# Kernel optimization log

Hardware: AMD Instinct MI355X
Metric: run time of the kernel (lower is better)

Reference implementation:

```python
import jax, jax.numpy as jnp
import numpy as np

B, T, DMODEL, H, DK, DV, FF = 4, 1024, 1024, 16, 64, 64, 4096


def _weight_mask(dmodel, dk):
    # tril ones -> 0 on/below diag, -inf above (matches torch masked_fill)
    m = jnp.tril(jnp.ones((dmodel, dk), dtype=jnp.float32))
    return jnp.where(m == 0, -jnp.inf, 0.0).astype(jnp.float32)


def _mha(Q, K, V, Wq, Wk, Wv, Wo, maskout):
    dk = Wq.shape[-1]
    if maskout:
        mask = _weight_mask(Wq.shape[1], dk)[None]  # (1, dmodel, dk)
        # softmax over the dmodel axis of the masked weight tensors (axis -2)
        Wq = jax.nn.softmax(Wq + mask, axis=-2)
        Wk = jax.nn.softmax(Wk + mask, axis=-2)
    WqQ = jnp.einsum('btd,hdk->bhtk', Q, Wq)
    WkK = jnp.einsum('btd,hdk->bhtk', K, Wk)
    WvV = jnp.einsum('btd,hdv->bhtv', V, Wv)
    scores = jnp.einsum('bhtk,bhsk->bhts', WqQ, WkK) / jnp.sqrt(jnp.float32(dk))
    # NOTE: source softmaxes over axis -2 (the QUERY axis), not the key axis
    attn = jax.nn.softmax(scores, axis=-2)
    out = jnp.einsum('bhts,bhsv->bhtv', attn, WvV)
    b, h, t, dv = out.shape
    out = out.transpose(0, 2, 1, 3).reshape(b, t, h * dv)  # (B, T, dmodel)
    return out @ Wo


def _norm(x):
    mean = jnp.mean(x, axis=-1, keepdims=True)
    std = jnp.std(x, axis=-1, keepdims=True, ddof=1)  # torch.std is unbiased
    return (x - mean) / std


def setup_inputs() -> dict:
    key = jax.random.key(0)
    ks = jax.random.split(key, 14)
    s = 0.02
    return {
        'x': jax.random.normal(ks[0], (B, T, DMODEL), jnp.float32),
        'y': jax.random.normal(ks[1], (B, T, DMODEL), jnp.float32),
        'Wq1': jax.random.normal(ks[2], (H, DMODEL, DK), jnp.float32) * s,
        'Wk1': jax.random.normal(ks[3], (H, DMODEL, DK), jnp.float32) * s,
        'Wv1': jax.random.normal(ks[4], (H, DMODEL, DV), jnp.float32) * s,
        'Wo1': jax.random.normal(ks[5], (DMODEL, DMODEL), jnp.float32) * s,
        'Wq2': jax.random.normal(ks[6], (H, DMODEL, DK), jnp.float32) * s,
        'Wk2': jax.random.normal(ks[7], (H, DMODEL, DK), jnp.float32) * s,
        'Wv2': jax.random.normal(ks[8], (H, DMODEL, DV), jnp.float32) * s,
        'Wo2': jax.random.normal(ks[9], (DMODEL, DMODEL), jnp.float32) * s,
        'w_in': jax.random.normal(ks[10], (FF, DMODEL), jnp.float32) * s,
        'b_in': jax.random.normal(ks[11], (FF,), jnp.float32) * s,
        'w_out': jax.random.normal(ks[12], (DMODEL, FF), jnp.float32) * s,
        'b_out': jax.random.normal(ks[13], (DMODEL,), jnp.float32) * s,
    }


def reference(x, y, Wq1, Wk1, Wv1, Wo1, Wq2, Wk2, Wv2, Wo2, w_in, b_in, w_out, b_out):
    # masked self-attention on decoded seq y
    out1 = _norm(_mha(y, y, y, Wq1, Wk1, Wv1, Wo1, True) + y)
    # cross-attention against encoded seq x
    out2 = _norm(_mha(out1, x, x, Wq2, Wk2, Wv2, Wo2, False) + out1)
    ff = jax.nn.relu(out2 @ w_in.T + b_in) @ w_out.T + b_out
    out3 = _norm(ff + out2)
    return (x, out3)
```

## Files before the change

kernel.cpp:

```cpp
#include <hip/hip_runtime.h>
#include <hip/hip_bf16.h>

#define BB 4
#define TT 1024
#define DD 1024
#define HH 16
#define DKK 64
#define FFF 4096

typedef unsigned short u16;
typedef unsigned int u32;
typedef __attribute__((ext_vector_type(8))) short s16x8;
typedef __attribute__((ext_vector_type(4))) float f32x4;

static __device__ __forceinline__ float bf2f(u16 s) {
  union { u32 u; float f; } v; v.u = ((u32)s) << 16; return v.f;
}
static __device__ __forceinline__ u16 f2bf(float f) {
  union { float f; u32 u; } v; v.f = f;
  u32 r = v.u + 0x7FFFu + ((v.u >> 16) & 1u);
  return (u16)(r >> 16);
}

#define GLDS(gp, lp) __builtin_amdgcn_global_load_lds( \
    (const __attribute__((address_space(1))) u32*)(gp), \
    (__attribute__((address_space(3))) u32*)(lp), 16, 0, 0)

static __device__ __forceinline__ void swz_block(int& bx, int& by) {
  int gx = gridDim.x, gy = gridDim.y;
  int nwg = gx * gy;
  int orig = by * gx + bx;
  int q = nwg >> 3, r = nwg & 7;
  int xcd = orig & 7, sl = orig >> 3;
  int wgid = (xcd < r ? xcd * (q + 1) : r * (q + 1) + (xcd - r) * q) + sl;
  int g = gx << 3;
  int grp = wgid / g, rem = wgid % g;
  bx = rem >> 3;
  by = (grp << 3) + (rem & 7);
}

static __device__ __forceinline__ void swz_attn(int& tileIdx, int& bh) {
  int orig = blockIdx.y * 8 + blockIdx.x;
  int wgid = ((orig & 7) << 6) | (orig >> 3);
  tileIdx = wgid & 7;
  bh = wgid >> 3;
}

__global__ __launch_bounds__(256) void k_f2bf(const float* __restrict__ s, u16* __restrict__ d, int n) {
  int i = (blockIdx.x * 256 + threadIdx.x) * 4;
  if (i < n) {
    float4 v = *(const float4*)(s + i);
    u16 o[4] = { f2bf(v.x), f2bf(v.y), f2bf(v.z), f2bf(v.w) };
    *(ushort4*)(d + i) = *(ushort4*)o;
  }
}

__global__ __launch_bounds__(256) void k_combine_bf(const u16* __restrict__ a, const u16* __restrict__ b,
                                                    u16* __restrict__ d, int n) {
  int i = (blockIdx.x * 256 + threadIdx.x) * 4;
  if (i < n) {
    ushort4 va = *(const ushort4*)(a + i);
    ushort4 vb = *(const ushort4*)(b + i);
    u16 o[4] = { f2bf(bf2f(va.x) + bf2f(vb.x)), f2bf(bf2f(va.y) + bf2f(vb.y)),
                 f2bf(bf2f(va.z) + bf2f(vb.z)), f2bf(bf2f(va.w) + bf2f(vb.w)) };
    *(ushort4*)(d + i) = *(ushort4*)o;
  }
}

__global__ __launch_bounds__(256) void k_xprep(const float* __restrict__ x, float* __restrict__ dout,
                                               u16* __restrict__ xb, int n) {
  int i = (blockIdx.x * 256 + threadIdx.x) * 4;
  if (i < n) {
    float4 v = *(const float4*)(x + i);
    *(float4*)(dout + i) = v;
    u16 o[4] = { f2bf(v.x), f2bf(v.y), f2bf(v.z), f2bf(v.w) };
    *(ushort4*)(xb + i) = *(ushort4*)o;
  }
}

__global__ __launch_bounds__(256) void k_softmax_w_bf(const float* __restrict__ W, u16* __restrict__ Bt) {
  int col = blockIdx.x;
  int h = col >> 6, k = col & 63;
  int tid = threadIdx.x;
  const float* w = W + ((size_t)h * DD) * DKK + k;
  __shared__ float red[256];
  float m = -1e30f;
  for (int d = k + tid; d < DD; d += 256) m = fmaxf(m, w[(size_t)d * DKK]);
  red[tid] = m; __syncthreads();
  for (int s = 128; s > 0; s >>= 1) { if (tid < s) red[tid] = fmaxf(red[tid], red[tid + s]); __syncthreads(); }
  m = red[0]; __syncthreads();
  float sum = 0.f;
  for (int d = k + tid; d < DD; d += 256) sum += __expf(w[(size_t)d * DKK] - m);
  red[tid] = sum; __syncthreads();
  for (int s = 128; s > 0; s >>= 1) { if (tid < s) red[tid] += red[tid + s]; __syncthreads(); }
  float inv = 1.f / red[0];
  for (int d = tid; d < DD; d += 256) {
    float v = (d >= k) ? __expf(w[(size_t)d * DKK] - m) * inv : 0.f;
    Bt[(size_t)col * DD + d] = f2bf(v);
  }
}

__global__ __launch_bounds__(256) void k_reorder_w_bf(const float* __restrict__ W, u16* __restrict__ Bt) {
  int d0 = blockIdx.x << 6, h = blockIdx.y;
  __shared__ float t[64][65];
  int tid = threadIdx.x;
  const float* src = W + (size_t)h * DD * DKK + (size_t)d0 * DKK;
  #pragma unroll
  for (int i = 0; i < 16; ++i) {
    int e = i * 256 + tid; int r = e >> 6, c = e & 63;
    t[r][c] = src[(size_t)r * DKK + c];
  }
  __syncthreads();
  #pragma unroll
  for (int i = 0; i < 16; ++i) {
    int e = i * 256 + tid; int c = e >> 6, r = e & 63;
    Bt[((size_t)(h * 64 + c)) * DD + d0 + r] = f2bf(t[r][c]);
  }
}

__global__ __launch_bounds__(256) void k_transpose_bf(const float* __restrict__ W, u16* __restrict__ Bt) {
  int k0 = blockIdx.x << 6, n0 = blockIdx.y << 6;
  __shared__ float t[64][65];
  int tid = threadIdx.x;
  #pragma unroll
  for (int i = 0; i < 16; ++i) {
    int e = i * 256 + tid; int r = e >> 6, c = e & 63;
    t[r][c] = W[(size_t)(k0 + r) * DD + n0 + c];
  }
  __syncthreads();
  #pragma unroll
  for (int i = 0; i < 16; ++i) {
    int e = i * 256 + tid; int c = e >> 6, r = e & 63;
    Bt[(size_t)(n0 + c) * DD + k0 + r] = f2bf(t[r][c]);
  }
}

__global__ __launch_bounds__(512) void k_mfma_nt(
    const u16* __restrict__ A, const u16* __restrict__ B,
    u16* __restrict__ P0, u16* __restrict__ P1, u16* __restrict__ P2, u16* __restrict__ P3,
    u16* __restrict__ Cb, u16* __restrict__ Cb2, u16* __restrict__ Ct,
    const float* __restrict__ bias, int relu, int mode, int M, int N, int K) {
  __shared__ u16 SLDS[24576];
  int bx = blockIdx.x, by = blockIdx.y;
  swz_block(bx, by);
  int tid = threadIdx.x, wave = tid >> 6, lane = tid & 63;
  int row0 = by << 7, col0 = bx << 7;
  int wm = (wave >> 2) << 6;
  int wn = (wave & 3) << 5;

  int Ksl = K / gridDim.z;
  int kbase = blockIdx.z * Ksl;
  int nt = Ksl >> 5;

  f32x4 acc[4][2];
  #pragma unroll
  for (int m = 0; m < 4; ++m)
    #pragma unroll
    for (int n = 0; n < 2; ++n) acc[m][n] = f32x4{0.f, 0.f, 0.f, 0.f};

  int srow = tid >> 2, scol = (tid & 3) << 3;
  const u16* Ag = A + (size_t)(row0 + srow) * K + scol;
  const u16* Bg = B + (size_t)(col0 + srow) * K + scol;
  int wbase = wave << 9;

  int fr = lane & 15, kg = (lane >> 4) << 3;
  int ardo = (wm + fr) * 32 + kg;
  int brdo = 12288 + (wn + fr) * 32 + kg;

  auto STAGE = [&](int buf, int k0) {
    GLDS(Ag + k0, SLDS + buf * 4096 + wbase);
    GLDS(Bg + k0, SLDS + 12288 + buf * 4096 + wbase);
  };

  STAGE(0, kbase);
  if (nt > 1) STAGE(1, kbase + 32);
  int bufT = 0;
  for (int t = 0; t < nt; ++t) {
    if (t + 1 < nt) asm volatile("s_waitcnt vmcnt(2)" ::: "memory");
    else            asm volatile("s_waitcnt vmcnt(0)" ::: "memory");
    __builtin_amdgcn_s_barrier();
    asm volatile("" ::: "memory");
    if (t + 2 < nt) {
      int b2 = bufT + 2; if (b2 >= 3) b2 -= 3;
      STAGE(b2, kbase + (t + 2) * 32);
    }
    const u16* Ard = SLDS + bufT * 4096 + ardo;
    const u16* Brd = SLDS + bufT * 4096 + brdo;
    s16x8 aF[4], bF[2];
    #pragma unroll
    for (int m = 0; m < 4; ++m) aF[m] = *(const s16x8*)(Ard + m * 16 * 32);
    #pragma unroll
    for (int n = 0; n < 2; ++n) bF[n] = *(const s16x8*)(Brd + n * 16 * 32);
    #pragma unroll
    for (int m = 0; m < 4; ++m)
      #pragma unroll
      for (int n = 0; n < 2; ++n)
        acc[m][n] = __builtin_amdgcn_mfma_f32_16x16x32_bf16(aF[m], bF[n], acc[m][n], 0, 0, 0);
    ++bufT; if (bufT == 3) bufT = 0;
  }
  __syncthreads();

  int fq = (lane >> 4) << 2;

  u16* dstRow = nullptr; u16* dstCol = nullptr;
  int rowPitch = 1024, colBase = col0 & 1023;
  if (mode == 0) {
    rowPitch = N; colBase = col0;
    if (gridDim.z > 1) {
      int z = blockIdx.z;
      dstRow = (z == 0) ? P0 : ((z == 1) ? P1 : ((z == 2) ? P2 : P3));
    } else dstRow = Cb;
  }
  else if (mode == 1) { int q = col0 >> 10; if (q == 0) dstRow = Cb; else if (q == 1) dstRow = Cb2; else dstCol = Ct; }
  else { int q = col0 >> 10; if (q == 0) dstRow = Cb; else dstCol = Ct; }

  u16* Ep = SLDS + wave * 2048;
  #pragma unroll
  for (int m = 0; m < 4; ++m) {
    #pragma unroll
    for (int n = 0; n < 2; ++n) {
      int col = col0 + wn + n * 16 + fr;
      float bs = bias ? bias[col] : 0.f;
      #pragma unroll
      for (int r = 0; r < 4; ++r) {
        float v = acc[m][n][r] + bs;
        if (relu) v = fmaxf(v, 0.f);
        Ep[(fq + r) * 40 + n * 16 + fr] = f2bf(v);
      }
    }
    if (dstRow) {
      int rw = lane >> 2, seg = lane & 3;
      const u16* src = Ep + rw * 40 + seg * 8;
      u16* gd = dstRow + (size_t)(row0 + wm + m * 16 + rw) * rowPitch + colBase + wn + seg * 8;
      *(uint4*)gd = *(const uint4*)src;
    } else {
      int c = lane >> 1, half = lane & 1;
      u16 tmp[8];
      #pragma unroll
      for (int j = 0; j < 8; ++j) tmp[j] = Ep[(half * 8 + j) * 40 + c];
      u16* gd = dstCol + (size_t)(colBase + wn + c) * 4096 + row0 + wm + m * 16 + half * 8;
      *(uint4*)gd = *(const uint4*)tmp;
    }
  }
}

static __device__ __forceinline__ void stage_tile512(const u16* __restrict__ g, int gp, u16* L, int tid) {
  int row = tid >> 3, col8 = (tid & 7) << 3;
  *(uint4*)(L + row * 72 + col8) = *(const uint4*)(g + (size_t)row * gp + col8);
}

__global__ __launch_bounds__(512) void k_attn_stats_mfma(const u16* __restrict__ Qb, const u16* __restrict__ Kb,
                                                         float* __restrict__ csum) {
  __shared__ u16 Ks[2 * 4608];
  __shared__ u16 Qs[4608];
  int tid = threadIdx.x, wave = tid >> 6, lane = tid & 63;
  int tileIdx, bh;
  swz_attn(tileIdx, bh);
  int b = bh >> 4, h = bh & 15;
  int s0 = tileIdx << 7;
  int tile = wave >> 2, sw = wave & 3;
  stage_tile512(Kb + ((size_t)(b * TT + s0)) * DD + h * 64, DD, Ks, tid);
  stage_tile512(Kb + ((size_t)(b * TT + s0 + 64)) * DD + h * 64, DD, Ks + 4608, tid);
  int row = tid >> 3, col8 = (tid & 7) << 3;
  const u16* Qg = Qb + ((size_t)(b * TT) + row) * DD + h * 64 + col8;
  uint4 qreg = *(const uint4*)Qg;
  __syncthreads();
  int fr = lane & 15, g = lane >> 4;
  const u16* Bbase = Ks + tile * 4608 + (sw * 16 + fr) * 72 + g * 8;
  const u16* Abase = Qs + fr * 72 + g * 8;
  s16x8 bF0 = *(const s16x8*)(Bbase);
  s16x8 bF1 = *(const s16x8*)(Bbase + 32);
  float sum = 0.f;
  for (int t0 = 0; t0 < TT; t0 += 64) {
    __syncthreads();
    *(uint4*)(Qs + row * 72 + col8) = qreg;
    __syncthreads();
    if (t0 + 64 < TT) qreg = *(const uint4*)(Qg + (size_t)(t0 + 64) * DD);
    #pragma unroll
    for (int mt = 0; mt < 4; ++mt) {
      f32x4 acc = f32x4{0.f, 0.f, 0.f, 0.f};
      s16x8 a0 = *(const s16x8*)(Abase + mt * 16 * 72);
      s16x8 a1 = *(const s16x8*)(Abase + mt * 16 * 72 + 32);
      acc = __builtin_amdgcn_mfma_f32_16x16x32_bf16(a0, bF0, acc, 0, 0, 0);
      acc = __builtin_amdgcn_mfma_f32_16x16x32_bf16(a1, bF1, acc, 0, 0, 0);
      sum += __expf(acc[0] * 0.125f) + __expf(acc[1] * 0.125f)
           + __expf(acc[2] * 0.125f) + __expf(acc[3] * 0.125f);
    }
  }
  sum += __shfl_xor(sum, 16, 64);
  sum += __shfl_xor(sum, 32, 64);
  if (lane < 16) csum[(size_t)bh * TT + s0 + tile * 64 + sw * 16 + lane] = sum;
}

__global__ __launch_bounds__(512) void k_attn_apply_mfma(const u16* __restrict__ Qb, const u16* __restrict__ Kb,
                                                         const u16* __restrict__ Vt,
                                                         const float* __restrict__ csum,
                                                         u16* __restrict__ Op) {
  __shared__ u16 Qs[2 * 4608];
  __shared__ u16 KV2[2 * 4608];
  __shared__ u16 Pl[8 * 1024];
  __shared__ float rcsL[64];
  u16* Ks = KV2;
  u16* VTs = KV2 + 4608;
  int tid = threadIdx.x, wave = tid >> 6, lane = tid & 63;
  int tileIdx, bh;
  swz_attn(tileIdx, bh);
  int b = bh >> 4, h = bh & 15;
  int t0 = tileIdx << 7;
  int tile = wave >> 2, tw = wave & 3;
  stage_tile512(Qb + ((size_t)(b * TT + t0)) * DD + h * 64, DD, Qs, tid);
  stage_tile512(Qb + ((size_t)(b * TT + t0 + 64)) * DD + h * 64, DD, Qs + 4608, tid);
  int row = tid >> 3, col8 = (tid & 7) << 3;
  const u16* Kg = Kb + ((size_t)(b * TT) + row) * DD + h * 64 + col8;
  const u16* Vg = Vt + ((size_t)(h * 64) + row) * 4096 + (size_t)b * TT + col8;
  const size_t cbase = (size_t)bh * TT;
  uint4 kreg = *(const uint4*)Kg;
  uint4 vreg = *(const uint4*)Vg;
  float rc0 = (tid < 64) ? csum[cbase + tid] : 0.f;
  __syncthreads();
  int fr = lane & 15, g = lane >> 4;
  const u16* QbF = Qs + tile * 4608 + (tw * 16 + fr) * 72 + g * 8;
  const u16* KaF = Ks + fr * 72 + g * 8;
  char* Pw = (char*)(Pl + wave * 1024);
  uint swz = ((uint)(lane & 7)) << 4;
  s16x8 qF0 = *(const s16x8*)(QbF);
  s16x8 qF1 = *(const s16x8*)(QbF + 32);
  f32x4 acc_o[4];
  #pragma unroll
  for (int nt = 0; nt < 4; ++nt) acc_o[nt] = f32x4{0.f, 0.f, 0.f, 0.f};

  for (int s0 = 0; s0 < TT; s0 += 64) {
    __syncthreads();
    *(uint4*)(Ks + row * 72 + col8) = kreg;
    *(uint4*)(VTs + row * 72 + col8) = vreg;
    if (tid < 64) rcsL[tid] = 1.f / rc0;
    __syncthreads();
    if (s0 + 64 < TT) {
      kreg = *(const uint4*)(Kg + (size_t)(s0 + 64) * DD);
      vreg = *(const uint4*)(Vg + s0 + 64);
      if (tid < 64) rc0 = csum[cbase + s0 + 64 + tid];
    }
    #pragma unroll
    for (int mt = 0; mt < 4; ++mt) {
      f32x4 acc = f32x4{0.f, 0.f, 0.f, 0.f};
      s16x8 a0 = *(const s16x8*)(KaF + mt * 16 * 72);
      s16x8 a1 = *(const s16x8*)(KaF + mt * 16 * 72 + 32);
      acc = __builtin_amdgcn_mfma_f32_16x16x32_bf16(a0, qF0, acc, 0, 0, 0);
      acc = __builtin_amdgcn_mfma_f32_16x16x32_bf16(a1, qF1, acc, 0, 0, 0);
      f32x4 rc4 = *(const f32x4*)&rcsL[mt * 16 + g * 4];
      u16 pb[4];
      #pragma unroll
      for (int r = 0; r < 4; ++r)
        pb[r] = f2bf(__expf(acc[r] * 0.125f) * rc4[r]);
      uint woff = (uint)fr * 128 + (uint)(mt * 16 + g * 4) * 2;
      uint2 wv; wv.x = (u32)pb[0] | ((u32)pb[1] << 16); wv.y = (u32)pb[2] | ((u32)pb[3] << 16);
      *(uint2*)(Pw + (woff ^ swz)) = wv;
    }
    uint rbase = (uint)fr * 128;
    s16x8 pF0 = *(const s16x8*)(Pw + ((rbase + g * 16) ^ swz));
    s16x8 pF1 = *(const s16x8*)(Pw + ((rbase + 64 + g * 16) ^ swz));
    #pragma unroll
    for (int nt = 0; nt < 4; ++nt) {
      s16x8 v0 = *(const s16x8*)(VTs + (nt * 16 + fr) * 72 + g * 8);
      s16x8 v1 = *(const s16x8*)(VTs + (nt * 16 + fr) * 72 + 32 + g * 8);
      acc_o[nt] = __builtin_amdgcn_mfma_f32_16x16x32_bf16(pF0, v0, acc_o[nt], 0, 0, 0);
      acc_o[nt] = __builtin_amdgcn_mfma_f32_16x16x32_bf16(pF1, v1, acc_o[nt], 0, 0, 0);
    }
  }
  __syncthreads();
  u16* Ep = KV2 + wave * 1088;
  #pragma unroll
  for (int nt = 0; nt < 4; ++nt)
    #pragma unroll
    for (int r = 0; r < 4; ++r)
      Ep[(g * 4 + r) * 68 + nt * 16 + fr] = f2bf(acc_o[nt][r]);
  {
    int rw = lane >> 2, seg = lane & 3;
    const u16* src = Ep + rw * 68 + seg * 16;
    u16* gd = Op + ((size_t)(b * TT + t0 + tile * 64 + tw * 16 + rw)) * DD + h * 64 + seg * 16;
    #pragma unroll
    for (int i = 0; i < 4; ++i) *(uint2*)(gd + i * 4) = *(const uint2*)(src + i * 4);
  }
}

__global__ __launch_bounds__(256) void k_add_norm(const u16* __restrict__ A, const u16* __restrict__ A2,
                                                  const u16* __restrict__ A3, const u16* __restrict__ A4,
                                                  const float* __restrict__ bias,
                                                  const float* __restrict__ Bv,
                                                  float* __restrict__ O, u16* __restrict__ Ob) {
  int row = blockIdx.x, tid = threadIdx.x;
  size_t base = (size_t)row * DD;
  int c0 = tid * 4;
  __shared__ float red[256];
  float v[4];
  {
    ushort4 a = *(const ushort4*)(A + base + c0);
    float4 bv = *(const float4*)(Bv + base + c0);
    v[0] = bf2f(a.x) + bv.x; v[1] = bf2f(a.y) + bv.y;
    v[2] = bf2f(a.z) + bv.z; v[3] = bf2f(a.w) + bv.w;
  }
  if (A2) {
    ushort4 a = *(const ushort4*)(A2 + base + c0);
    v[0] += bf2f(a.x); v[1] += bf2f(a.y); v[2] += bf2f(a.z); v[3] += bf2f(a.w);
  }
  if (A3) {
    ushort4 a = *(const ushort4*)(A3 + base + c0);
    v[0] += bf2f(a.x); v[1] += bf2f(a.y); v[2] += bf2f(a.z); v[3] += bf2f(a.w);
  }
  if (A4) {
    ushort4 a = *(const ushort4*)(A4 + base + c0);
    v[0] += bf2f(a.x); v[1] += bf2f(a.y); v[2] += bf2f(a.z); v[3] += bf2f(a.w);
  }
  if (bias) {
    float4 bs = *(const float4*)(bias + c0);
    v[0] += bs.x; v[1] += bs.y; v[2] += bs.z; v[3] += bs.w;
  }
  float s = v[0] + v[1] + v[2] + v[3];
  red[tid] = s; __syncthreads();
  for (int t = 128; t > 0; t >>= 1) { if (tid < t) red[tid] += red[tid + t]; __syncthreads(); }
  float mean = red[0] * (1.f / 1024.f);
  __syncthreads();
  float vs = 0.f;
  #pragma unroll
  for (int i = 0; i < 4; ++i) { float d = v[i] - mean; vs += d * d; }
  red[tid] = vs; __syncthreads();
  for (int t = 128; t > 0; t >>= 1) { if (tid < t) red[tid] += red[tid + t]; __syncthreads(); }
  float inv = rsqrtf(red[0] * (1.f / 1023.f));
  float o[4];
  #pragma unroll
  for (int i = 0; i < 4; ++i) o[i] = (v[i] - mean) * inv;
  *(float4*)(O + base + c0) = *(float4*)o;
  if (Ob) {
    u16 ob[4] = { f2bf(o[0]), f2bf(o[1]), f2bf(o[2]), f2bf(o[3]) };
    *(ushort4*)(Ob + base + c0) = *(ushort4*)ob;
  }
}

extern "C" void kernel_launch(void* const* d_in, const int* in_sizes, int n_in,
                              void* d_out, int out_size, void* d_ws, size_t ws_size,
                              hipStream_t stream) {
  (void)in_sizes; (void)n_in; (void)out_size; (void)ws_size;
  const float* x    = (const float*)d_in[0];
  const float* y    = (const float*)d_in[1];
  const float* Wq1  = (const float*)d_in[2];
  const float* Wk1  = (const float*)d_in[3];
  const float* Wv1  = (const float*)d_in[4];
  const float* Wo1  = (const float*)d_in[5];
  const float* Wq2  = (const float*)d_in[6];
  const float* Wk2  = (const float*)d_in[7];
  const float* Wv2  = (const float*)d_in[8];
  const float* Wo2  = (const float*)d_in[9];
  const float* w_in  = (const float*)d_in[10];
  const float* b_in  = (const float*)d_in[11];
  const float* w_out = (const float*)d_in[12];
  const float* b_out = (const float*)d_in[13];

  float* ws = (float*)d_ws;
  size_t off = 0;
  auto allocw = [&](size_t nw) { float* p = ws + off; off += nw; return p; };
  const size_t MR = (size_t)BB * TT;
  const size_t ND = MR * DD;

  u16* Bq   = (u16*)allocw(512 * 1024);
  u16* Bk   = (u16*)allocw(512 * 1024);
  u16* Bv   = (u16*)allocw(512 * 1024);
  u16* Bwo  = (u16*)allocw(512 * 1024);
  u16* Wi   = (u16*)allocw(2 * 1024 * 1024);
  u16* Wob  = (u16*)allocw(2 * 1024 * 1024);
  u16* xbf  = (u16*)allocw(ND / 2);
  u16* ybf  = (u16*)allocw(ND / 2);
  u16* REG  = (u16*)allocw(ND * 2);
  float* ff2  = allocw(ND);
  float* out1 = allocw(ND);
  float* out2 = allocw(ND);
  float* csum = allocw((size_t)BB * HH * TT);

  u16* Qb = REG;
  u16* Kb = REG + ND;
  u16* Vt = REG + 2 * ND;
  u16* Mb = REG + 3 * ND;
  u16* ff1b = REG;
  u16* out2bf = ybf;
  float* doutHi = (float*)d_out + ND;
  u16* p0 = (u16*)ff2;
  u16* p1 = (u16*)ff2 + ND;
  u16* p2 = (u16*)out1;
  u16* p3 = (u16*)out1 + ND;

  dim3 blk(256), blkG(512), blkA(512);
  dim3 gConv(4096);
  dim3 gSm(1024);
  dim3 gRw(16, 16);
  dim3 gQKV(24, 32);
  dim3 gKV(16, 32);
  dim3 gP2(8, 32, 2);
  dim3 gF1(32, 32);
  dim3 gFF2(8, 32, 4);
  dim3 gAttn(8, 64);
  dim3 gNorm(MR);

  k_xprep<<<gConv, blk, 0, stream>>>(x, (float*)d_out, xbf, (int)ND);
  k_f2bf<<<gConv, blk, 0, stream>>>(y, ybf, (int)ND);
  k_f2bf<<<gConv, blk, 0, stream>>>(w_in, Wi, FFF * DD);
  k_f2bf<<<gConv, blk, 0, stream>>>(w_out, Wob, DD * FFF);

  k_softmax_w_bf<<<gSm, blk, 0, stream>>>(Wq1, Bq);
  k_softmax_w_bf<<<gSm, blk, 0, stream>>>(Wk1, Bk);
  k_reorder_w_bf<<<gRw, blk, 0, stream>>>(Wv1, Bv);
  k_transpose_bf<<<gRw, blk, 0, stream>>>(Wo1, Bwo);
  k_mfma_nt<<<gQKV, blkG, 0, stream>>>(ybf, Bq, nullptr, nullptr, nullptr, nullptr, Qb, Kb, Vt, nullptr, 0, 1, 4096, 3072, 1024);
  k_attn_stats_mfma<<<gAttn, blkA, 0, stream>>>(Qb, Kb, csum);
  k_attn_apply_mfma<<<gAttn, blkA, 0, stream>>>(Qb, Kb, Vt, csum, Mb);
  k_mfma_nt<<<gP2, blkG, 0, stream>>>(Mb, Bwo, p0, p1, nullptr, nullptr, nullptr, nullptr, nullptr, nullptr, 0, 0, 4096, 1024, 1024);
  k_add_norm<<<gNorm, blk, 0, stream>>>(p0, p1, nullptr, nullptr, nullptr, y, out1, Mb );

  k_reorder_w_bf<<<gRw, blk, 0, stream>>>(Wq2, Bq);
  k_reorder_w_bf<<<gRw, blk, 0, stream>>>(Wk2, Bk);
  k_reorder_w_bf<<<gRw, blk, 0, stream>>>(Wv2, Bv);
  k_transpose_bf<<<gRw, blk, 0, stream>>>(Wo2, Bwo);
  k_mfma_nt<<<gP2, blkG, 0, stream>>>(Mb , Bq, p0, p1, nullptr, nullptr, nullptr, nullptr, nullptr, nullptr, 0, 0, 4096, 1024, 1024);
  k_combine_bf<<<gConv, blk, 0, stream>>>(p0, p1, Qb, (int)ND);
  k_mfma_nt<<<gKV, blkG, 0, stream>>>(xbf, Bk, nullptr, nullptr, nullptr, nullptr, Kb, nullptr, Vt, nullptr, 0, 2, 4096, 2048, 1024);
  k_attn_stats_mfma<<<gAttn, blkA, 0, stream>>>(Qb, Kb, csum);
  k_attn_apply_mfma<<<gAttn, blkA, 0, stream>>>(Qb, Kb, Vt, csum, Mb);
  k_mfma_nt<<<gP2, blkG, 0, stream>>>(Mb, Bwo, p0, p1, nullptr, nullptr, nullptr, nullptr, nullptr, nullptr, 0, 0, 4096, 1024, 1024);
  k_add_norm<<<gNorm, blk, 0, stream>>>(p0, p1, nullptr, nullptr, nullptr, out1, out2, out2bf);

  k_mfma_nt<<<gF1, blkG, 0, stream>>>(out2bf, Wi, nullptr, nullptr, nullptr, nullptr, ff1b, nullptr, nullptr, b_in, 1, 0, 4096, 4096, 1024);
  k_mfma_nt<<<gFF2, blkG, 0, stream>>>(ff1b, Wob, p0, p1, p2, p3, nullptr, nullptr, nullptr, nullptr, 0, 0, 4096, 1024, 4096);
  k_add_norm<<<gNorm, blk, 0, stream>>>(p0, p1, p2, p3, b_out, out2, doutHi, nullptr);
}
```

Baseline: 403.6 us.

## Merge prep kernels and fuse cross-attention Q/K/V projections into one GEMM

Folds the four fp32-to-bf16 conversion launches into one segmented kernel, and does the same for the two weight softmaxes and the three weight reorders. The cross-attention Q projection, which was a split-K GEMM followed by a combine kernel, is merged with the K/V projection into a single mode-1 GEMM launch. That launch picks its A operand per column block: out1 bf16 for Q, x bf16 for K and V. This removes several launches, the partial-sum round trip and the combine kernel. The cost is a per-block operand selection and the assumption that Bq, Bk and Bv are contiguous.

```diff
diff --git a/kernel.cpp b/kernel.cpp
--- a/kernel.cpp
+++ b/kernel.cpp
@@ -46,40 +46,33 @@
   bh = wgid >> 3;
 }
 
-__global__ __launch_bounds__(256) void k_f2bf(const float* __restrict__ s, u16* __restrict__ d, int n) {
-  int i = (blockIdx.x * 256 + threadIdx.x) * 4;
-  if (i < n) {
-    float4 v = *(const float4*)(s + i);
-    u16 o[4] = { f2bf(v.x), f2bf(v.y), f2bf(v.z), f2bf(v.w) };
-    *(ushort4*)(d + i) = *(ushort4*)o;
-  }
-}
-
-__global__ __launch_bounds__(256) void k_combine_bf(const u16* __restrict__ a, const u16* __restrict__ b,
-                                                    u16* __restrict__ d, int n) {
-  int i = (blockIdx.x * 256 + threadIdx.x) * 4;
-  if (i < n) {
-    ushort4 va = *(const ushort4*)(a + i);
-    ushort4 vb = *(const ushort4*)(b + i);
-    u16 o[4] = { f2bf(bf2f(va.x) + bf2f(vb.x)), f2bf(bf2f(va.y) + bf2f(vb.y)),
-                 f2bf(bf2f(va.z) + bf2f(vb.z)), f2bf(bf2f(va.w) + bf2f(vb.w)) };
-    *(ushort4*)(d + i) = *(ushort4*)o;
-  }
-}
-
-__global__ __launch_bounds__(256) void k_xprep(const float* __restrict__ x, float* __restrict__ dout,
-                                               u16* __restrict__ xb, int n) {
-  int i = (blockIdx.x * 256 + threadIdx.x) * 4;
-  if (i < n) {
+__global__ __launch_bounds__(256) void k_prep(const float* __restrict__ x, float* __restrict__ dout,
+                                              u16* __restrict__ xb,
+                                              const float* __restrict__ y, u16* __restrict__ yb,
+                                              const float* __restrict__ wi, u16* __restrict__ Wi,
+                                              const float* __restrict__ wo, u16* __restrict__ Wob) {
+  int seg = blockIdx.x >> 12;
+  int i = ((blockIdx.x & 4095) * 256 + threadIdx.x) * 4;
+  if (seg == 0) {
     float4 v = *(const float4*)(x + i);
     *(float4*)(dout + i) = v;
     u16 o[4] = { f2bf(v.x), f2bf(v.y), f2bf(v.z), f2bf(v.w) };
     *(ushort4*)(xb + i) = *(ushort4*)o;
-  }
-}
-
-__global__ __launch_bounds__(256) void k_softmax_w_bf(const float* __restrict__ W, u16* __restrict__ Bt) {
-  int col = blockIdx.x;
+    return;
+  }
+  const float* s = (seg == 1) ? y : ((seg == 2) ? wi : wo);
+  u16* d = (seg == 1) ? yb : ((seg == 2) ? Wi : Wob);
+  float4 v = *(const float4*)(s + i);
+  u16 o[4] = { f2bf(v.x), f2bf(v.y), f2bf(v.z), f2bf(v.w) };
+  *(ushort4*)(d + i) = *(ushort4*)o;
+}
+
+__global__ __launch_bounds__(256) void k_softmax_w2_bf(const float* __restrict__ Wq, const float* __restrict__ Wk,
+                                                       u16* __restrict__ Bq, u16* __restrict__ Bk) {
+  int sel = blockIdx.x >> 10;
+  int col = blockIdx.x & 1023;
+  const float* W = sel ? Wk : Wq;
+  u16* Bt = sel ? Bk : Bq;
   int h = col >> 6, k = col & 63;
   int tid = threadIdx.x;
   const float* w = W + ((size_t)h * DD) * DKK + k;
@@ -100,6 +93,28 @@
   }
 }
 
+__global__ __launch_bounds__(256) void k_reorder3_bf(const float* __restrict__ W0, const float* __restrict__ W1,
+                                                     const float* __restrict__ W2, u16* __restrict__ Bt0) {
+  int z = blockIdx.z;
+  const float* W = (z == 0) ? W0 : ((z == 1) ? W1 : W2);
+  u16* Bt = Bt0 + (size_t)z * 1024 * 1024;
+  int d0 = blockIdx.x << 6, h = blockIdx.y;
+  __shared__ float t[64][65];
+  int tid = threadIdx.x;
+  const float* src = W + (size_t)h * DD * DKK + (size_t)d0 * DKK;
+  #pragma unroll
+  for (int i = 0; i < 16; ++i) {
+    int e = i * 256 + tid; int r = e >> 6, c = e & 63;
+    t[r][c] = src[(size_t)r * DKK + c];
+  }
+  __syncthreads();
+  #pragma unroll
+  for (int i = 0; i < 16; ++i) {
+    int e = i * 256 + tid; int c = e >> 6, r = e & 63;
+    Bt[((size_t)(h * 64 + c)) * DD + d0 + r] = f2bf(t[r][c]);
+  }
+}
+
 __global__ __launch_bounds__(256) void k_reorder_w_bf(const float* __restrict__ W, u16* __restrict__ Bt) {
   int d0 = blockIdx.x << 6, h = blockIdx.y;
   __shared__ float t[64][65];
@@ -136,7 +151,8 @@
 }
 
 __global__ __launch_bounds__(512) void k_mfma_nt(
-    const u16* __restrict__ A, const u16* __restrict__ B,
+    const u16* __restrict__ A, const u16* __restrict__ A2,
+    const u16* __restrict__ B,
     u16* __restrict__ P0, u16* __restrict__ P1, u16* __restrict__ P2, u16* __restrict__ P3,
     u16* __restrict__ Cb, u16* __restrict__ Cb2, u16* __restrict__ Ct,
     const float* __restrict__ bias, int relu, int mode, int M, int N, int K) {
@@ -148,6 +164,8 @@
   int wm = (wave >> 2) << 6;
   int wn = (wave & 3) << 5;
 
+  const u16* Asrc = (mode == 1 && A2 && (col0 >> 10) > 0) ? A2 : A;
+
   int Ksl = K / gridDim.z;
   int kbase = blockIdx.z * Ksl;
   int nt = Ksl >> 5;
@@ -159,7 +177,7 @@
     for (int n = 0; n < 2; ++n) acc[m][n] = f32x4{0.f, 0.f, 0.f, 0.f};
 
   int srow = tid >> 2, scol = (tid & 3) << 3;
-  const u16* Ag = A + (size_t)(row0 + srow) * K + scol;
+  const u16* Ag = Asrc + (size_t)(row0 + srow) * K + scol;
   const u16* Bg = B + (size_t)(col0 + srow) * K + scol;
   int wbase = wave << 9;
 
@@ -486,47 +504,40 @@
   u16* p1 = (u16*)ff2 + ND;
   u16* p2 = (u16*)out1;
   u16* p3 = (u16*)out1 + ND;
+  (void)Bv;
 
   dim3 blk(256), blkG(512), blkA(512);
-  dim3 gConv(4096);
-  dim3 gSm(1024);
+  dim3 gPrep(16384);
+  dim3 gSm2(2048);
   dim3 gRw(16, 16);
+  dim3 gRw3(16, 16, 3);
   dim3 gQKV(24, 32);
-  dim3 gKV(16, 32);
   dim3 gP2(8, 32, 2);
   dim3 gF1(32, 32);
   dim3 gFF2(8, 32, 4);
   dim3 gAttn(8, 64);
   dim3 gNorm(MR);
 
-  k_xprep<<<gConv, blk, 0, stream>>>(x, (float*)d_out, xbf, (int)ND);
-  k_f2bf<<<gConv, blk, 0, stream>>>(y, ybf, (int)ND);
-  k_f2bf<<<gConv, blk, 0, stream>>>(w_in, Wi, FFF * DD);
-  k_f2bf<<<gConv, blk, 0, stream>>>(w_out, Wob, DD * FFF);
-
-  k_softmax_w_bf<<<gSm, blk, 0, stream>>>(Wq1, Bq);
-  k_softmax_w_bf<<<gSm, blk, 0, stream>>>(Wk1, Bk);
+  k_prep<<<gPrep, blk, 0, stream>>>(x, (float*)d_out, xbf, y, ybf, w_in, Wi, w_out, Wob);
+
+  k_softmax_w2_bf<<<gSm2, blk, 0, stream>>>(Wq1, Wk1, Bq, Bk);
   k_reorder_w_bf<<<gRw, blk, 0, stream>>>(Wv1, Bv);
   k_transpose_bf<<<gRw, blk, 0, stream>>>(Wo1, Bwo);
-  k_mfma_nt<<<gQKV, blkG, 0, stream>>>(ybf, Bq, nullptr, nullptr, nullptr, nullptr, Qb, Kb, Vt, nullptr, 0, 1, 4096, 3072, 1024);
+  k_mfma_nt<<<gQKV, blkG, 0, stream>>>(ybf, nullptr, Bq, nullptr, nullptr, nullptr, nullptr, Qb, Kb, Vt, nullptr, 0, 1, 4096, 3072, 1024);
   k_attn_stats_mfma<<<gAttn, blkA, 0, stream>>>(Qb, Kb, csum);
   k_attn_apply_mfma<<<gAttn, blkA, 0, stream>>>(Qb, Kb, Vt, csum, Mb);
-  k_mfma_nt<<<gP2, blkG, 0, stream>>>(Mb, Bwo, p0, p1, nullptr, nullptr, nullptr, nullptr, nullptr, nullptr, 0, 0, 4096, 1024, 1024);
+  k_mfma_nt<<<gP2, blkG, 0, stream>>>(Mb, nullptr, Bwo, p0, p1, nullptr, nullptr, nullptr, nullptr, nullptr, nullptr, 0, 0, 4096, 1024, 1024);
   k_add_norm<<<gNorm, blk, 0, stream>>>(p0, p1, nullptr, nullptr, nullptr, y, out1, Mb );
 
-  k_reorder_w_bf<<<gRw, blk, 0, stream>>>(Wq2, Bq);
-  k_reorder_w_bf<<<gRw, blk, 0, stream>>>(Wk2, Bk);
-  k_reorder_w_bf<<<gRw, blk, 0, stream>>>(Wv2, Bv);
+  k_reorder3_bf<<<gRw3, blk, 0, stream>>>(Wq2, Wk2, Wv2, Bq);
   k_transpose_bf<<<gRw, blk, 0, stream>>>(Wo2, Bwo);
-  k_mfma_nt<<<gP2, blkG, 0, stream>>>(Mb , Bq, p0, p1, nullptr, nullptr, nullptr, nullptr, nullptr, nullptr, 0, 0, 4096, 1024, 1024);
-  k_combine_bf<<<gConv, blk, 0, stream>>>(p0, p1, Qb, (int)ND);
-  k_mfma_nt<<<gKV, blkG, 0, stream>>>(xbf, Bk, nullptr, nullptr, nullptr, nullptr, Kb, nullptr, Vt, nullptr, 0, 2, 4096, 2048, 1024);
+  k_mfma_nt<<<gQKV, blkG, 0, stream>>>(Mb, xbf, Bq, nullptr, nullptr, nullptr, nullptr, Qb, Kb, Vt, nullptr, 0, 1, 4096, 3072, 1024);
   k_attn_stats_mfma<<<gAttn, blkA, 0, stream>>>(Qb, Kb, csum);
   k_attn_apply_mfma<<<gAttn, blkA, 0, stream>>>(Qb, Kb, Vt, csum, Mb);
-  k_mfma_nt<<<gP2, blkG, 0, stream>>>(Mb, Bwo, p0, p1, nullptr, nullptr, nullptr, nullptr, nullptr, nullptr, 0, 0, 4096, 1024, 1024);
+  k_mfma_nt<<<gP2, blkG, 0, stream>>>(Mb, nullptr, Bwo, p0, p1, nullptr, nullptr, nullptr, nullptr, nullptr, nullptr, 0, 0, 4096, 1024, 1024);
   k_add_norm<<<gNorm, blk, 0, stream>>>(p0, p1, nullptr, nullptr, nullptr, out1, out2, out2bf);
 
-  k_mfma_nt<<<gF1, blkG, 0, stream>>>(out2bf, Wi, nullptr, nullptr, nullptr, nullptr, ff1b, nullptr, nullptr, b_in, 1, 0, 4096, 4096, 1024);
-  k_mfma_nt<<<gFF2, blkG, 0, stream>>>(ff1b, Wob, p0, p1, p2, p3, nullptr, nullptr, nullptr, nullptr, 0, 0, 4096, 1024, 4096);
+  k_mfma_nt<<<gF1, blkG, 0, stream>>>(out2bf, nullptr, Wi, nullptr, nullptr, nullptr, nullptr, ff1b, nullptr, nullptr, b_in, 1, 0, 4096, 4096, 1024);
+  k_mfma_nt<<<gFF2, blkG, 0, stream>>>(ff1b, nullptr, Wob, p0, p1, p2, p3, nullptr, nullptr, nullptr, nullptr, 0, 0, 4096, 1024, 4096);
   k_add_norm<<<gNorm, blk, 0, stream>>>(p0, p1, p2, p3, b_out, out2, doutHi, nullptr);
 }
```

Result: faster. 385.4 us (-4.5%).
